# Kernel tuning notes

Hardware: AMD Instinct MI355X
Metric: run time of the kernel (lower is better)

Reference implementation:

```python
import jax, jax.numpy as jnp
import numpy as np

B, S, D = 8, 1024, 1024
H, DK = 16, 64  # num_heads, d_k; H*DK == D
NEG_INF = 1e29


def setup_inputs() -> dict:
    key = jax.random.key(0)
    ks = jax.random.split(key, 12)
    sc = 1.0 / np.sqrt(D)
    q = jax.random.normal(ks[0], (B, S, D), jnp.float32)
    k = jax.random.normal(ks[1], (B, S, D), jnp.float32)
    v = jax.random.normal(ks[2], (B, S, D), jnp.float32)
    # causal mask, broadcast per batch (mask==0 positions are masked out)
    mask = jnp.broadcast_to(jnp.tril(jnp.ones((S, S), jnp.int32)), (B, S, S))
    Wq = jax.random.normal(ks[3], (D, D), jnp.float32) * sc
    bq = jax.random.normal(ks[4], (D,), jnp.float32) * 0.01
    Wk = jax.random.normal(ks[5], (D, D), jnp.float32) * sc
    bk = jax.random.normal(ks[6], (D,), jnp.float32) * 0.01
    Wv = jax.random.normal(ks[7], (D, D), jnp.float32) * sc
    bv = jax.random.normal(ks[8], (D,), jnp.float32) * 0.01
    Wo = jax.random.normal(ks[9], (D, D), jnp.float32) * sc
    bo = jax.random.normal(ks[10], (D,), jnp.float32) * 0.01
    return {"q": q, "k": k, "v": v, "mask": mask,
            "Wq": Wq, "bq": bq, "Wk": Wk, "bk": bk,
            "Wv": Wv, "bv": bv, "Wo": Wo, "bo": bo}


def reference(q, k, v, mask, Wq, bq, Wk, bk, Wv, bv, Wo, bo):
    # Linear projections (torch Linear: x @ W.T + b)
    q1 = q @ Wq.T + bq
    k1 = k @ Wk.T + bk
    v1 = v @ Wv.T + bv
    # [B, S, D] -> [B, H, S, DK]
    def split_heads(x):
        return x.reshape(B, S, H, DK).transpose(0, 2, 1, 3)
    q3, k3, v3 = split_heads(q1), split_heads(k1), split_heads(v1)
    # scores [B, H, S, S]
    scores = jnp.einsum('bhqd,bhkd->bhqk', q3, k3) / jnp.sqrt(jnp.float32(DK))
    scores = jnp.where(mask[:, None, :, :] == 0, -NEG_INF, scores)
    probs = jax.nn.softmax(scores, axis=-1)
    attn = jnp.einsum('bhqk,bhkd->bhqd', probs, v3)  # [B, H, S, DK]
    out = attn.transpose(0, 2, 1, 3).reshape(B, S, D)
    return out @ Wo.T + bo
```

## Files before the change

kernel.cpp:

```cpp
#include <hip/hip_runtime.h>
#include <hip/hip_bf16.h>
#include <stdint.h>

constexpr int NB = 8;
constexpr int NS = 1024;
constexpr int ND = 1024;
constexpr int NH = 16;
constexpr int NDK = 64;
constexpr int NKT = ND / 64;

typedef __bf16 bf16_t;
typedef __attribute__((ext_vector_type(8))) __bf16 bf16x8;
typedef __attribute__((ext_vector_type(4))) __bf16 bf16x4;
typedef __attribute__((ext_vector_type(4))) float f32x4;
typedef __attribute__((ext_vector_type(16))) float f32x16;

#define GLL16(g, s) __builtin_amdgcn_global_load_lds( \
    (const __attribute__((address_space(1))) void*)(g), \
    (__attribute__((address_space(3))) void*)(s), 16, 0, 0)

__device__ __forceinline__ unsigned cvtpk_bf16(float lo, float hi) {
  unsigned r;
  asm("v_cvt_pk_bf16_f32 %0, %1, %2" : "=v"(r) : "v"(lo), "v"(hi));
  return r;
}

__device__ __forceinline__ void cvt_body(const float* __restrict__ s,
                                         bf16_t* __restrict__ d, long n) {
  long i0 = (long)(blockIdx.x * blockDim.x + threadIdx.x) * 4;
  long step = (long)gridDim.x * blockDim.x * 4;
  for (long i = i0; i < n; i += step) {
    float4 f = *(const float4*)(s + i);
    bf16x4 o;
    o[0] = (bf16_t)f.x; o[1] = (bf16_t)f.y; o[2] = (bf16_t)f.z; o[3] = (bf16_t)f.w;
    *(bf16x4*)(d + i) = o;
  }
}

__global__ __launch_bounds__(256) void cvt4_kernel(const float* s0, bf16_t* d0,
                                                   const float* s1, bf16_t* d1,
                                                   const float* s2, bf16_t* d2,
                                                   const float* s3, bf16_t* d3, long n) {
  const float* s = blockIdx.y == 0 ? s0 : blockIdx.y == 1 ? s1 : blockIdx.y == 2 ? s2 : s3;
  bf16_t* d = blockIdx.y == 0 ? d0 : blockIdx.y == 1 ? d1 : blockIdx.y == 2 ? d2 : d3;
  cvt_body(s, d, n);
}

__global__ __launch_bounds__(256, 2) void gemm_qkv(
    const float* A0, const bf16_t* W0, const float* b0, bf16_t* C0,
    const float* A1, const bf16_t* W1, const float* b1, bf16_t* C1,
    const float* A2, const bf16_t* W2, const float* b2, bf16_t* C2) {
  __shared__ bf16_t S[5 * 8192];
  const int o = blockIdx.x;
  const int xcd = o & 7, s = o >> 3;
  const int bx = s & 7, u = s >> 3;
  const int zby = xcd + 8 * u;
  const int z = zby >> 6, by = zby & 63;
  const float* A = z == 0 ? A0 : z == 1 ? A1 : A2;
  const bf16_t* W = z == 0 ? W0 : z == 1 ? W1 : W2;
  const float* bb = z == 0 ? b0 : z == 1 ? b1 : b2;
  bf16_t* C = z == 0 ? C0 : z == 1 ? C1 : C2;

  const int tid = threadIdx.x;
  const int l = tid & 63, w = tid >> 6;
  const int wr = w >> 1, wc = w & 1;
  const int g = l >> 4, r = l & 15;
  const int m0 = by * 128, n0 = bx * 128;
  const int wbase = w * 512;

  bf16_t* Ab = S;
  bf16_t* Bb = S + 16384;

  float4 faA[8], faB[8];
  auto issueA = [&](int t, float4 (&dst)[8]) {
#pragma unroll
    for (int it = 0; it < 4; ++it) {
      const float* p = A + (size_t)(m0 + it * 32 + (tid >> 3)) * ND + t * 64 + (tid & 7) * 8;
      dst[it * 2]     = *(const float4*)p;
      dst[it * 2 + 1] = *(const float4*)(p + 4);
    }
  };
  auto writeA = [&](int ab, float4 (&src)[8]) {
#pragma unroll
    for (int it = 0; it < 4; ++it) {
      int row = it * 32 + (tid >> 3), c = tid & 7;
      bf16x8 ov;
      ov[0] = (bf16_t)src[it * 2].x;     ov[1] = (bf16_t)src[it * 2].y;
      ov[2] = (bf16_t)src[it * 2].z;     ov[3] = (bf16_t)src[it * 2].w;
      ov[4] = (bf16_t)src[it * 2 + 1].x; ov[5] = (bf16_t)src[it * 2 + 1].y;
      ov[6] = (bf16_t)src[it * 2 + 1].z; ov[7] = (bf16_t)src[it * 2 + 1].w;
      *(bf16x8*)(Ab + ab * 8192 + row * 64 + ((c ^ (row & 7)) << 3)) = ov;
    }
  };
  auto stageB = [&](int qb, int t) {
#pragma unroll
    for (int it = 0; it < 4; ++it) {
      int idx = it * 256 + tid;
      int row = idx >> 3, c = (idx & 7) ^ (row & 7);
      GLL16(W + (size_t)(n0 + row) * ND + (t << 6) + c * 8,
            Bb + qb * 8192 + it * 2048 + wbase);
    }
  };

  f32x4 acc[4][4] = {};

  issueA(0, faA);
  issueA(1, faB);
  stageB(0, 0);
  stageB(1, 1);
  asm volatile("s_waitcnt vmcnt(4)" ::: "memory");
  __builtin_amdgcn_sched_barrier(0);
  writeA(0, faA);
  asm volatile("s_waitcnt lgkmcnt(0)" ::: "memory");
  __builtin_amdgcn_s_barrier();

  auto bodyT = [&](int t, float4 (&fiss)[8], float4 (&fwr)[8]) {
    if (t + 2 < NKT) issueA(t + 2, fiss);
    __builtin_amdgcn_sched_barrier(0);
    if (t + 2 < NKT) stageB((t + 2) % 3, t + 2);
    __builtin_amdgcn_sched_barrier(0);

    const bf16_t* a_ = Ab + (t & 1) * 8192;
    const bf16_t* b_ = Bb + (t % 3) * 8192;
#pragma unroll
    for (int kk = 0; kk < 2; ++kk) {
      bf16x8 af[4], bw[4];
#pragma unroll
      for (int m = 0; m < 4; ++m) {
        int row = wr * 64 + m * 16 + r;
        af[m] = *(const bf16x8*)(a_ + row * 64 + (((kk * 4 + g) ^ (row & 7)) << 3));
      }
#pragma unroll
      for (int n = 0; n < 4; ++n) {
        int row = wc * 64 + n * 16 + r;
        bw[n] = *(const bf16x8*)(b_ + row * 64 + (((kk * 4 + g) ^ (row & 7)) << 3));
      }
      __builtin_amdgcn_s_setprio(1);
#pragma unroll
      for (int m = 0; m < 4; ++m)
#pragma unroll
        for (int n = 0; n < 4; ++n)
          acc[m][n] = __builtin_amdgcn_mfma_f32_16x16x32_bf16(af[m], bw[n], acc[m][n], 0, 0, 0);
      __builtin_amdgcn_s_setprio(0);
    }

    if (t + 2 < NKT)      asm volatile("s_waitcnt vmcnt(12)" ::: "memory");
    else                  asm volatile("s_waitcnt vmcnt(0)" ::: "memory");
    __builtin_amdgcn_sched_barrier(0);
    if (t + 1 < NKT) writeA((t + 1) & 1, fwr);
    asm volatile("s_waitcnt lgkmcnt(0)" ::: "memory");
    __builtin_amdgcn_s_barrier();
  };

#pragma unroll 1
  for (int tt = 0; tt < NKT; tt += 2) {
    bodyT(tt, faA, faB);
    bodyT(tt + 1, faB, faA);
  }

  if (z == 2) {
#pragma unroll
    for (int n = 0; n < 4; ++n) {
      int col = n0 + wc * 64 + n * 16 + r;
      int hh = col >> 6, dk = col & 63;
      float bv = bb[col];
#pragma unroll
      for (int m = 0; m < 4; ++m) {
        int row0 = m0 + wr * 64 + m * 16 + g * 4;
        int b_ = row0 >> 10, s0 = row0 & 1023;
        bf16x4 o4;
#pragma unroll
        for (int j = 0; j < 4; ++j) o4[j] = (bf16_t)(acc[m][n][j] + bv);
        *(bf16x4*)(C + (((size_t)b_ * 16 + hh) * 64 + dk) * 1024 + s0) = o4;
      }
    }
  } else {
#pragma unroll
    for (int n = 0; n < 4; ++n) {
      int col = n0 + wc * 64 + n * 16 + r;
      float bv = bb[col];
#pragma unroll
      for (int m = 0; m < 4; ++m) {
        int row0 = m0 + wr * 64 + m * 16 + g * 4;
#pragma unroll
        for (int j = 0; j < 4; ++j)
          C[(size_t)(row0 + j) * ND + col] = (bf16_t)(acc[m][n][j] + bv);
      }
    }
  }
}

__global__ __launch_bounds__(512, 2) void gemm_bt(const bf16_t* __restrict__ A,
                                                  const bf16_t* __restrict__ W,
                                                  const float* __restrict__ bias,
                                                  float* __restrict__ Cout,
                                                  int M, int N, int K) {
  __shared__ bf16_t S[3 * 24576];
  const int o = blockIdx.x;
  const int xcd = o & 7, s = o >> 3;
  const int bx = s & 7, u = s >> 3;
  const int by = xcd + 8 * u;

  const int tid = threadIdx.x;
  const int l = tid & 63, w = tid >> 6;
  const int wr = w >> 1, wc = w & 1;
  const int g = l >> 4, r = l & 15;
  const int m0 = by * 256, n0 = bx * 128;
  const int wbase = w * 512;

  auto stageA2 = [&](int q, int t, int half) {
#pragma unroll
    for (int it = half * 2; it < half * 2 + 2; ++it) {
      int idx = it * 512 + tid;
      int row = idx >> 3, c = (idx & 7) ^ (row & 7);
      GLL16(A + (size_t)(m0 + row) * K + (t << 6) + c * 8,
            S + q * 24576 + it * 4096 + wbase);
    }
  };
  auto stageB2 = [&](int q, int t) {
#pragma unroll
    for (int it = 0; it < 2; ++it) {
      int idx = it * 512 + tid;
      int row = idx >> 3, c = (idx & 7) ^ (row & 7);
      GLL16(W + (size_t)(n0 + row) * K + (t << 6) + c * 8,
            S + q * 24576 + 16384 + it * 4096 + wbase);
    }
  };

  f32x4 acc[4][4] = {};
  const int NKT2 = K >> 6;

  stageA2(0, 0, 0); stageA2(0, 0, 1); stageB2(0, 0);
  stageA2(1, 1, 0); stageA2(1, 1, 1); stageB2(1, 1);

  int q = 0;
  for (int t = 0; t < NKT2; ++t) {
    const bool pf = (t + 2 < NKT2);
    int q2 = q + 2; if (q2 >= 3) q2 -= 3;

    if (t + 1 < NKT2) asm volatile("s_waitcnt vmcnt(6)" ::: "memory");
    else              asm volatile("s_waitcnt vmcnt(0)" ::: "memory");
    __builtin_amdgcn_s_barrier();

    const bf16_t* a_ = S + q * 24576;
    const bf16_t* b_ = a_ + 16384;

#pragma unroll
    for (int kk = 0; kk < 2; ++kk) {
      bf16x8 bw[4];
#pragma unroll
      for (int n = 0; n < 4; ++n) {
        int row = wc * 64 + n * 16 + r;
        bw[n] = *(const bf16x8*)(b_ + row * 64 + (((kk * 4 + g) ^ (row & 7)) << 3));
      }
#pragma unroll
      for (int mh = 0; mh < 2; ++mh) {
        bf16x8 af[2];
#pragma unroll
        for (int i = 0; i < 2; ++i) {
          int row = wr * 64 + (mh * 2 + i) * 16 + r;
          af[i] = *(const bf16x8*)(a_ + row * 64 + (((kk * 4 + g) ^ (row & 7)) << 3));
        }
        if (pf) {
          int ph = kk * 2 + mh;
          if (ph == 0)      stageA2(q2, t + 2, 0);
          else if (ph == 1) stageA2(q2, t + 2, 1);
          else if (ph == 2) stageB2(q2, t + 2);
        }
        __builtin_amdgcn_s_barrier();
        asm volatile("s_waitcnt lgkmcnt(0)" ::: "memory");
        __builtin_amdgcn_sched_barrier(0);
        __builtin_amdgcn_s_setprio(1);
#pragma unroll
        for (int i = 0; i < 2; ++i)
#pragma unroll
          for (int n = 0; n < 4; ++n)
            acc[mh * 2 + i][n] = __builtin_amdgcn_mfma_f32_16x16x32_bf16(
                af[i], bw[n], acc[mh * 2 + i][n], 0, 0, 0);
        __builtin_amdgcn_s_setprio(0);
        __builtin_amdgcn_sched_barrier(0);
      }
    }
    ++q; if (q >= 3) q -= 3;
  }

#pragma unroll
  for (int n = 0; n < 4; ++n) {
    int col = n0 + wc * 64 + n * 16 + r;
    float bv = bias[col];
#pragma unroll
    for (int m = 0; m < 4; ++m) {
      int row0 = m0 + wr * 64 + m * 16 + g * 4;
#pragma unroll
      for (int j = 0; j < 4; ++j)
        Cout[(size_t)(row0 + j) * N + col] = acc[m][n][j] + bv;
    }
  }
}

__global__ __launch_bounds__(256, 2) void attn_kernel(const bf16_t* __restrict__ Q1,
                                                      const bf16_t* __restrict__ K1,
                                                      const bf16_t* __restrict__ V1t,
                                                      bf16_t* __restrict__ attn) {
  __shared__ bf16_t Kt[2][64 * 64];
  __shared__ bf16_t Vt[2][64 * 64];

  const int tid = threadIdx.x;
  const int l = tid & 63, w = tid >> 6;
  const int q32 = l & 31, h5 = l >> 5;

  const int o = blockIdx.x;
  const int os = (o & 7) * 64 + (o >> 3);
  const int pair = os & 3, hb = os >> 2;
  const int h = hb & 15, b = hb >> 4;

  constexpr float SC = 0.18033688011112042f;
  const bf16_t* vbase = V1t + ((size_t)(b * 16 + h) * 64) * 1024;

  auto stageKV = [&](int kt2, int pb) {
    const int k0 = kt2 * 64;
#pragma unroll
    for (int it = 0; it < 2; ++it) {
      int idx = it * 256 + tid;
      int row = idx >> 3, c = (idx & 7) ^ (row & 7);
      GLL16(K1 + ((size_t)b * NS + k0 + row) * ND + h * 64 + c * 8,
            &Kt[pb][it * 2048 + w * 512]);
      GLL16(vbase + (size_t)row * 1024 + k0 + c * 8,
            &Vt[pb][it * 2048 + w * 512]);
    }
  };

  for (int ph = 0; ph < 2; ++ph) {
    const int qt = ph ? (7 - pair) : pair;
    const int qrow_g = qt * 128 + w * 32 + q32;

    const bf16_t* qptr = Q1 + ((size_t)b * NS + qrow_g) * ND + h * 64;
    bf16x8 qf[4];
#pragma unroll
    for (int ds = 0; ds < 4; ++ds) {
      qf[ds] = *(const bf16x8*)(qptr + ds * 16 + h5 * 8);
#pragma unroll
      for (int i = 0; i < 8; ++i) qf[ds][i] = (bf16_t)((float)qf[ds][i] * SC);
    }

    float mrun = -1e30f, lrun = 0.f;
    f32x16 oacc0 = {}, oacc1 = {};

    __syncthreads();

    const int nkt = 2 * qt + 2;
    stageKV(0, 0);

    for (int kt = 0; kt < nkt; ++kt) {
      const int p = kt & 1;
      const int k0 = kt * 64;

      __syncthreads();

      if (kt + 1 < nkt) stageKV(kt + 1, p ^ 1);

      f32x16 s0 = {}, s1 = {};
      __builtin_amdgcn_s_setprio(1);
#pragma unroll
      for (int ds = 0; ds < 4; ++ds) {
        int dk2b = (ds * 16 + h5 * 8) * 2;
        {
          int row = q32;
          bf16x8 kf = *(const bf16x8*)((char*)Kt[p] + row * 128 + (dk2b ^ ((row & 7) << 4)));
          s0 = __builtin_amdgcn_mfma_f32_32x32x16_bf16(kf, qf[ds], s0, 0, 0, 0);
        }
        {
          int row = 32 + q32;
          bf16x8 kf = *(const bf16x8*)((char*)Kt[p] + row * 128 + (dk2b ^ ((row & 7) << 4)));
          s1 = __builtin_amdgcn_mfma_f32_32x32x16_bf16(kf, qf[ds], s1, 0, 0, 0);
        }
      }
      __builtin_amdgcn_s_setprio(0);

      if (kt >= 2 * qt) {
#pragma unroll
        for (int reg = 0; reg < 16; ++reg) {
          int key = k0 + (reg & 3) + 8 * (reg >> 2) + 4 * h5;
          if (key > qrow_g) s0[reg] = -1e30f;
          if (key + 32 > qrow_g) s1[reg] = -1e30f;
        }
      }

      float mx = s0[0];
#pragma unroll
      for (int i = 1; i < 16; ++i) mx = fmaxf(mx, s0[i]);
#pragma unroll
      for (int i = 0; i < 16; ++i) mx = fmaxf(mx, s1[i]);
      mx = fmaxf(mx, __shfl_xor(mx, 32));

      if (!__all(mx <= mrun + 8.0f)) {
        float m_new = fmaxf(mrun, mx);
        float esc = __builtin_amdgcn_exp2f(mrun - m_new);
        mrun = m_new;
        lrun *= esc;
#pragma unroll
        for (int i = 0; i < 16; ++i) { oacc0[i] *= esc; oacc1[i] *= esc; }
      }

      float rsum = 0.f;
#pragma unroll
      for (int i = 0; i < 16; ++i) { s0[i] = __builtin_amdgcn_exp2f(s0[i] - mrun); rsum += s0[i]; }
#pragma unroll
      for (int i = 0; i < 16; ++i) { s1[i] = __builtin_amdgcn_exp2f(s1[i] - mrun); rsum += s1[i]; }
      rsum += __shfl_xor(rsum, 32);
      lrun += rsum;

      bf16x8 pf[4];
#pragma unroll
      for (int ks = 0; ks < 4; ++ks) {
        const int base = (ks & 1) * 8;
        unsigned ca, cb, cc, cd;
        if (ks < 2) {
          ca = cvtpk_bf16(s0[base + 0], s0[base + 1]);
          cb = cvtpk_bf16(s0[base + 2], s0[base + 3]);
          cc = cvtpk_bf16(s0[base + 4], s0[base + 5]);
          cd = cvtpk_bf16(s0[base + 6], s0[base + 7]);
        } else {
          ca = cvtpk_bf16(s1[base + 0], s1[base + 1]);
          cb = cvtpk_bf16(s1[base + 2], s1[base + 3]);
          cc = cvtpk_bf16(s1[base + 4], s1[base + 5]);
          cd = cvtpk_bf16(s1[base + 6], s1[base + 7]);
        }
        asm volatile("v_permlane32_swap_b32 %0, %1" : "+v"(ca), "+v"(cc));
        asm volatile("v_permlane32_swap_b32 %0, %1" : "+v"(cb), "+v"(cd));
        union { unsigned u[4]; bf16x8 v; } pw;
        pw.u[0] = ca; pw.u[1] = cb; pw.u[2] = cc; pw.u[3] = cd;
        pf[ks] = pw.v;
      }

      __builtin_amdgcn_s_setprio(1);
#pragma unroll
      for (int ks = 0; ks < 4; ++ks) {
        int key2b = (ks * 16 + h5 * 8) * 2;
        {
          int row = q32;
          bf16x8 vf = *(const bf16x8*)((char*)Vt[p] + row * 128 + (key2b ^ ((row & 7) << 4)));
          oacc0 = __builtin_amdgcn_mfma_f32_32x32x16_bf16(vf, pf[ks], oacc0, 0, 0, 0);
        }
        {
          int row = 32 + q32;
          bf16x8 vf = *(const bf16x8*)((char*)Vt[p] + row * 128 + (key2b ^ ((row & 7) << 4)));
          oacc1 = __builtin_amdgcn_mfma_f32_32x32x16_bf16(vf, pf[ks], oacc1, 0, 0, 0);
        }
      }
      __builtin_amdgcn_s_setprio(0);
    }

    float linv = 1.0f / lrun;
    bf16_t* optr = attn + ((size_t)b * NS + qrow_g) * ND + h * 64;
#pragma unroll
    for (int rr = 0; rr < 4; ++rr) {
      bf16x4 o4a, o4b;
#pragma unroll
      for (int j = 0; j < 4; ++j) {
        o4a[j] = (bf16_t)(oacc0[rr * 4 + j] * linv);
        o4b[j] = (bf16_t)(oacc1[rr * 4 + j] * linv);
      }
      *(bf16x4*)(optr + rr * 8 + h5 * 4) = o4a;
      *(bf16x4*)(optr + 32 + rr * 8 + h5 * 4) = o4b;
    }
  }
}

extern "C" void kernel_launch(void* const* d_in, const int* in_sizes, int n_in,
                              void* d_out, int out_size, void* d_ws, size_t ws_size,
                              hipStream_t stream) {
  const float* q  = (const float*)d_in[0];
  const float* k  = (const float*)d_in[1];
  const float* v  = (const float*)d_in[2];
  const float* Wq = (const float*)d_in[4];
  const float* bq = (const float*)d_in[5];
  const float* Wk = (const float*)d_in[6];
  const float* bk = (const float*)d_in[7];
  const float* Wv = (const float*)d_in[8];
  const float* bv = (const float*)d_in[9];
  const float* Wo = (const float*)d_in[10];
  const float* bo = (const float*)d_in[11];
  float* out = (float*)d_out;

  const size_t NX = (size_t)NB * NS * ND;
  const size_t NW = (size_t)ND * ND;
  char* ws = (char*)d_ws;
  size_t off = 0;
  auto alloc = [&](size_t bytes) {
    char* p = ws + off;
    off += (bytes + 255) & ~(size_t)255;
    return p;
  };
  bf16_t* wqb = (bf16_t*)alloc(NW * 2);
  bf16_t* wkb = (bf16_t*)alloc(NW * 2);
  bf16_t* wvb = (bf16_t*)alloc(NW * 2);
  bf16_t* wob = (bf16_t*)alloc(NW * 2);
  bf16_t* q1  = (bf16_t*)alloc(NX * 2);
  bf16_t* k1  = (bf16_t*)alloc(NX * 2);
  bf16_t* v1t = (bf16_t*)alloc(NX * 2);
  bf16_t* at  = (bf16_t*)alloc(NX * 2);

  dim3 blk(256);
  cvt4_kernel<<<dim3(128, 4), blk, 0, stream>>>(Wq, wqb, Wk, wkb, Wv, wvb, Wo, wob, (long)NW);

  gemm_qkv<<<dim3(1536), dim3(256), 0, stream>>>(
      q, wqb, bq, q1, k, wkb, bk, k1, v, wvb, bv, v1t);

  attn_kernel<<<dim3(512), dim3(256), 0, stream>>>(q1, k1, v1t, at);

  gemm_bt<<<dim3(256), dim3(512), 0, stream>>>(at, wob, bo, out, NB * NS, ND, ND);
}
```

Baseline: 136.7 us.

## Deepen A-operand register prefetch to three stages and fully unroll K loop

The QKV projection GEMM now keeps three register buffers of fp32 A tiles in flight instead of two, issuing A loads three K-steps ahead. The bf16 conversion and LDS write of the next A tile move to before the MFMA block rather than after it. The K loop is fully unrolled so buffer indices become compile-time constants, with per-iteration vmcnt thresholds. The aim is to hide more global-load latency, at the cost of more VGPRs (possibly lower occupancy) and more code size.

```diff
diff --git a/kernel.cpp b/kernel.cpp
--- a/kernel.cpp
+++ b/kernel.cpp
@@ -71,24 +71,24 @@
   bf16_t* Ab = S;
   bf16_t* Bb = S + 16384;
 
-  float4 faA[8], faB[8];
-  auto issueA = [&](int t, float4 (&dst)[8]) {
+  float4 fa[3][8];
+  auto issueA = [&](int t, int buf) {
 #pragma unroll
     for (int it = 0; it < 4; ++it) {
       const float* p = A + (size_t)(m0 + it * 32 + (tid >> 3)) * ND + t * 64 + (tid & 7) * 8;
-      dst[it * 2]     = *(const float4*)p;
-      dst[it * 2 + 1] = *(const float4*)(p + 4);
-    }
-  };
-  auto writeA = [&](int ab, float4 (&src)[8]) {
+      fa[buf][it * 2]     = *(const float4*)p;
+      fa[buf][it * 2 + 1] = *(const float4*)(p + 4);
+    }
+  };
+  auto writeA = [&](int ab, int buf) {
 #pragma unroll
     for (int it = 0; it < 4; ++it) {
       int row = it * 32 + (tid >> 3), c = tid & 7;
       bf16x8 ov;
-      ov[0] = (bf16_t)src[it * 2].x;     ov[1] = (bf16_t)src[it * 2].y;
-      ov[2] = (bf16_t)src[it * 2].z;     ov[3] = (bf16_t)src[it * 2].w;
-      ov[4] = (bf16_t)src[it * 2 + 1].x; ov[5] = (bf16_t)src[it * 2 + 1].y;
-      ov[6] = (bf16_t)src[it * 2 + 1].z; ov[7] = (bf16_t)src[it * 2 + 1].w;
+      ov[0] = (bf16_t)fa[buf][it * 2].x;     ov[1] = (bf16_t)fa[buf][it * 2].y;
+      ov[2] = (bf16_t)fa[buf][it * 2].z;     ov[3] = (bf16_t)fa[buf][it * 2].w;
+      ov[4] = (bf16_t)fa[buf][it * 2 + 1].x; ov[5] = (bf16_t)fa[buf][it * 2 + 1].y;
+      ov[6] = (bf16_t)fa[buf][it * 2 + 1].z; ov[7] = (bf16_t)fa[buf][it * 2 + 1].w;
       *(bf16x8*)(Ab + ab * 8192 + row * 64 + ((c ^ (row & 7)) << 3)) = ov;
     }
   };
@@ -104,21 +104,30 @@
 
   f32x4 acc[4][4] = {};
 
-  issueA(0, faA);
-  issueA(1, faB);
   stageB(0, 0);
   stageB(1, 1);
-  asm volatile("s_waitcnt vmcnt(4)" ::: "memory");
+  issueA(0, 0);
+  issueA(1, 1);
+  issueA(2, 2);
+  asm volatile("s_waitcnt vmcnt(16)" ::: "memory");
   __builtin_amdgcn_sched_barrier(0);
-  writeA(0, faA);
+  writeA(0, 0);
   asm volatile("s_waitcnt lgkmcnt(0)" ::: "memory");
   __builtin_amdgcn_s_barrier();
 
-  auto bodyT = [&](int t, float4 (&fiss)[8], float4 (&fwr)[8]) {
-    if (t + 2 < NKT) issueA(t + 2, fiss);
-    __builtin_amdgcn_sched_barrier(0);
+#pragma unroll
+  for (int t = 0; t < NKT; ++t) {
     if (t + 2 < NKT) stageB((t + 2) % 3, t + 2);
     __builtin_amdgcn_sched_barrier(0);
+    if (t + 3 < NKT) issueA(t + 3, (t + 3) % 3);
+    __builtin_amdgcn_sched_barrier(0);
+
+    if (t <= 12)      asm volatile("s_waitcnt vmcnt(20)" ::: "memory");
+    else if (t == 13) asm volatile("s_waitcnt vmcnt(12)" ::: "memory");
+    else              asm volatile("s_waitcnt vmcnt(0)" ::: "memory");
+    __builtin_amdgcn_sched_barrier(0);
+
+    if (t + 1 < NKT) writeA((t + 1) & 1, (t + 1) % 3);
 
     const bf16_t* a_ = Ab + (t & 1) * 8192;
     const bf16_t* b_ = Bb + (t % 3) * 8192;
@@ -144,18 +153,8 @@
       __builtin_amdgcn_s_setprio(0);
     }
 
-    if (t + 2 < NKT)      asm volatile("s_waitcnt vmcnt(12)" ::: "memory");
-    else                  asm volatile("s_waitcnt vmcnt(0)" ::: "memory");
-    __builtin_amdgcn_sched_barrier(0);
-    if (t + 1 < NKT) writeA((t + 1) & 1, fwr);
     asm volatile("s_waitcnt lgkmcnt(0)" ::: "memory");
     __builtin_amdgcn_s_barrier();
-  };
-
-#pragma unroll 1
-  for (int tt = 0; tt < NKT; tt += 2) {
-    bodyT(tt, faA, faB);
-    bodyT(tt + 1, faB, faA);
   }
 
   if (z == 2) {
```

Result: slower. 140.9 us (+3.0%).

## Retile output GEMM to 128x128 blocks with split A/B prefetch buffering

Applied to the files above, without the earlier changes.

The output projection GEMM now runs 256-thread blocks on 128x128 tiles, with twice as many blocks as before. The old kernel staged A and B together in a single triple-buffered ring. Now A is double-buffered and B triple-buffered, each with its own prefetch distance, and only one barrier is taken per K step instead of several per sub-step. This is meant to cut synchronisation overhead and improve occupancy and load balance. In exchange, each block loses the reuse of B across 256 rows and the K-loop pipeline changes in a way that could expose load latency.

```diff
diff --git a/kernel.cpp b/kernel.cpp
--- a/kernel.cpp
+++ b/kernel.cpp
@@ -190,12 +190,11 @@
   }
 }
 
-__global__ __launch_bounds__(512, 2) void gemm_bt(const bf16_t* __restrict__ A,
+__global__ __launch_bounds__(256, 2) void gemm_bt(const bf16_t* __restrict__ A,
                                                   const bf16_t* __restrict__ W,
                                                   const float* __restrict__ bias,
-                                                  float* __restrict__ Cout,
-                                                  int M, int N, int K) {
-  __shared__ bf16_t S[3 * 24576];
+                                                  float* __restrict__ Cout) {
+  __shared__ bf16_t S[5 * 8192];
   const int o = blockIdx.x;
   const int xcd = o & 7, s = o >> 3;
   const int bx = s & 7, u = s >> 3;
@@ -205,83 +204,73 @@
   const int l = tid & 63, w = tid >> 6;
   const int wr = w >> 1, wc = w & 1;
   const int g = l >> 4, r = l & 15;
-  const int m0 = by * 256, n0 = bx * 128;
+  const int m0 = by * 128, n0 = bx * 128;
   const int wbase = w * 512;
 
-  auto stageA2 = [&](int q, int t, int half) {
-#pragma unroll
-    for (int it = half * 2; it < half * 2 + 2; ++it) {
-      int idx = it * 512 + tid;
+  bf16_t* Ab = S;
+  bf16_t* Bb = S + 16384;
+
+  auto stageA = [&](int qb, int t) {
+#pragma unroll
+    for (int it = 0; it < 4; ++it) {
+      int idx = it * 256 + tid;
       int row = idx >> 3, c = (idx & 7) ^ (row & 7);
-      GLL16(A + (size_t)(m0 + row) * K + (t << 6) + c * 8,
-            S + q * 24576 + it * 4096 + wbase);
-    }
-  };
-  auto stageB2 = [&](int q, int t) {
-#pragma unroll
-    for (int it = 0; it < 2; ++it) {
-      int idx = it * 512 + tid;
+      GLL16(A + (size_t)(m0 + row) * ND + (t << 6) + c * 8,
+            Ab + qb * 8192 + it * 2048 + wbase);
+    }
+  };
+  auto stageB = [&](int qb, int t) {
+#pragma unroll
+    for (int it = 0; it < 4; ++it) {
+      int idx = it * 256 + tid;
       int row = idx >> 3, c = (idx & 7) ^ (row & 7);
-      GLL16(W + (size_t)(n0 + row) * K + (t << 6) + c * 8,
-            S + q * 24576 + 16384 + it * 4096 + wbase);
+      GLL16(W + (size_t)(n0 + row) * ND + (t << 6) + c * 8,
+            Bb + qb * 8192 + it * 2048 + wbase);
     }
   };
 
   f32x4 acc[4][4] = {};
-  const int NKT2 = K >> 6;
-
-  stageA2(0, 0, 0); stageA2(0, 0, 1); stageB2(0, 0);
-  stageA2(1, 1, 0); stageA2(1, 1, 1); stageB2(1, 1);
-
-  int q = 0;
-  for (int t = 0; t < NKT2; ++t) {
-    const bool pf = (t + 2 < NKT2);
-    int q2 = q + 2; if (q2 >= 3) q2 -= 3;
-
-    if (t + 1 < NKT2) asm volatile("s_waitcnt vmcnt(6)" ::: "memory");
-    else              asm volatile("s_waitcnt vmcnt(0)" ::: "memory");
-    __builtin_amdgcn_s_barrier();
-
-    const bf16_t* a_ = S + q * 24576;
-    const bf16_t* b_ = a_ + 16384;
-
+
+  stageA(0, 0);
+  stageB(0, 0);
+  stageB(1, 1);
+  asm volatile("s_waitcnt vmcnt(4)" ::: "memory");
+  __builtin_amdgcn_s_barrier();
+
+  for (int t = 0; t < NKT; ++t) {
+    if (t + 1 < NKT) stageA((t + 1) & 1, t + 1);
+    __builtin_amdgcn_sched_barrier(0);
+    if (t + 2 < NKT) stageB((t + 2) % 3, t + 2);
+    __builtin_amdgcn_sched_barrier(0);
+
+    const bf16_t* a_ = Ab + (t & 1) * 8192;
+    const bf16_t* b_ = Bb + (t % 3) * 8192;
 #pragma unroll
     for (int kk = 0; kk < 2; ++kk) {
-      bf16x8 bw[4];
+      bf16x8 af[4], bw[4];
+#pragma unroll
+      for (int m = 0; m < 4; ++m) {
+        int row = wr * 64 + m * 16 + r;
+        af[m] = *(const bf16x8*)(a_ + row * 64 + (((kk * 4 + g) ^ (row & 7)) << 3));
+      }
 #pragma unroll
       for (int n = 0; n < 4; ++n) {
         int row = wc * 64 + n * 16 + r;
         bw[n] = *(const bf16x8*)(b_ + row * 64 + (((kk * 4 + g) ^ (row & 7)) << 3));
       }
-#pragma unroll
-      for (int mh = 0; mh < 2; ++mh) {
-        bf16x8 af[2];
-#pragma unroll
-        for (int i = 0; i < 2; ++i) {
-          int row = wr * 64 + (mh * 2 + i) * 16 + r;
-          af[i] = *(const bf16x8*)(a_ + row * 64 + (((kk * 4 + g) ^ (row & 7)) << 3));
-        }
-        if (pf) {
-          int ph = kk * 2 + mh;
-          if (ph == 0)      stageA2(q2, t + 2, 0);
-          else if (ph == 1) stageA2(q2, t + 2, 1);
-          else if (ph == 2) stageB2(q2, t + 2);
-        }
-        __builtin_amdgcn_s_barrier();
-        asm volatile("s_waitcnt lgkmcnt(0)" ::: "memory");
-        __builtin_amdgcn_sched_barrier(0);
-        __builtin_amdgcn_s_setprio(1);
-#pragma unroll
-        for (int i = 0; i < 2; ++i)
-#pragma unroll
-          for (int n = 0; n < 4; ++n)
-            acc[mh * 2 + i][n] = __builtin_amdgcn_mfma_f32_16x16x32_bf16(
-                af[i], bw[n], acc[mh * 2 + i][n], 0, 0, 0);
-        __builtin_amdgcn_s_setprio(0);
-        __builtin_amdgcn_sched_barrier(0);
-      }
-    }
-    ++q; if (q >= 3) q -= 3;
+      __builtin_amdgcn_s_setprio(1);
+#pragma unroll
+      for (int m = 0; m < 4; ++m)
+#pragma unroll
+        for (int n = 0; n < 4; ++n)
+          acc[m][n] = __builtin_amdgcn_mfma_f32_16x16x32_bf16(af[m], bw[n], acc[m][n], 0, 0, 0);
+      __builtin_amdgcn_s_setprio(0);
+    }
+
+    if (t + 2 < NKT) asm volatile("s_waitcnt vmcnt(4)" ::: "memory");
+    else             asm volatile("s_waitcnt vmcnt(0)" ::: "memory");
+    asm volatile("s_waitcnt lgkmcnt(0)" ::: "memory");
+    __builtin_amdgcn_s_barrier();
   }
 
 #pragma unroll
@@ -293,7 +282,7 @@
       int row0 = m0 + wr * 64 + m * 16 + g * 4;
 #pragma unroll
       for (int j = 0; j < 4; ++j)
-        Cout[(size_t)(row0 + j) * N + col] = acc[m][n][j] + bv;
+        Cout[(size_t)(row0 + j) * ND + col] = acc[m][n][j] + bv;
     }
   }
 }
@@ -509,5 +498,5 @@
 
   attn_kernel<<<dim3(512), dim3(256), 0, stream>>>(q1, k1, v1t, at);
 
-  gemm_bt<<<dim3(256), dim3(512), 0, stream>>>(at, wob, bo, out, NB * NS, ND, ND);
-}
+  gemm_bt<<<dim3(512), dim3(256), 0, stream>>>(at, wob, bo, out);
+}
```

Result: no change. 135.9 us (median of 2 runs) (-0.6%).
